# Performance work log

Hardware: AMD Instinct MI355X
Metric: run time of the kernel (lower is better)

## Reference

```python
import jax, jax.numpy as jnp
import numpy as np

B, S, E = 4, 2048, 1024


def setup_inputs() -> dict:
    key = jax.random.key(0)
    ks = jax.random.split(key, 7)
    sc = 1.0 / np.sqrt(E)
    return {
        "embedded": jax.random.normal(ks[0], (B, S, E), dtype=jnp.float32),
        "Wk": jax.random.normal(ks[1], (E, E), dtype=jnp.float32) * sc,
        "bk": jax.random.normal(ks[2], (E,), dtype=jnp.float32) * 0.01,
        "Wq": jax.random.normal(ks[3], (E, E), dtype=jnp.float32) * sc,
        "bq": jax.random.normal(ks[4], (E,), dtype=jnp.float32) * 0.01,
        "Wv": jax.random.normal(ks[5], (E, E), dtype=jnp.float32) * sc,
        "bv": jax.random.normal(ks[6], (E,), dtype=jnp.float32) * 0.01,
    }


def reference(embedded, Wk, bk, Wq, bq, Wv, bv):
    # embedded: [B, S, E]
    K = embedded @ Wk.T + bk  # [B,S,E]
    Q = embedded @ Wq.T + bq
    V = embedded @ Wv.T + bv
    seq_len = K.shape[1]
    # score[b,i,j] = K_i . Q_j, scaled by 1/sqrt(seq_len) (as in original)
    scores = jnp.einsum('bie,bje->bij', K, Q) / jnp.sqrt(jnp.asarray(seq_len, K.dtype))
    # softmax over dim=-2 -> over the key index i
    W = jax.nn.softmax(scores, axis=-2)  # [B,S,S]
    # Y = (V^T @ W)^T -> Y[b,j,d] = sum_i V[b,i,d] * W[b,i,j]
    Y = jnp.einsum('bid,bij->bjd', V, W)  # [B,S,E]
    return Y
```

## Files before the change

### kernel.cpp

```cpp
#include <hip/hip_runtime.h>
#include <hip/hip_bf16.h>


typedef __bf16 bf16x8 __attribute__((ext_vector_type(8)));
typedef float  f32x4  __attribute__((ext_vector_type(4)));

__device__ __forceinline__ unsigned short f2bf(float f) {
    unsigned int u = __float_as_uint(f);
    u = (u + 0x7FFFu + ((u >> 16) & 1u)) >> 16;
    return (unsigned short)u;
}

__global__ __launch_bounds__(256)
void cvt_all(const float* __restrict__ X,  const float* __restrict__ Wq,
             const float* __restrict__ Wk, const float* __restrict__ Wv,
             unsigned short* __restrict__ Xb,  unsigned short* __restrict__ Wqb,
             unsigned short* __restrict__ Wkb, unsigned short* __restrict__ Wvb,
             float* __restrict__ l) {
    long i = (long)blockIdx.x * 256 + threadIdx.x;
    if (i < 8192) l[i] = 0.0f;
    const float* src; unsigned short* dst; long off;
    if (i < 2097152L) { src = X; dst = Xb; off = i; }
    else {
        long j = i - 2097152L;
        int w = (int)(j >> 18);
        off = j & 262143L;
        src = (w == 0) ? Wq : (w == 1) ? Wk : Wv;
        dst = (w == 0) ? Wqb : (w == 1) ? Wkb : Wvb;
    }
    float4 v = reinterpret_cast<const float4*>(src)[off];
    ushort4 o;
    o.x = f2bf(v.x); o.y = f2bf(v.y); o.z = f2bf(v.z); o.w = f2bf(v.w);
    reinterpret_cast<ushort4*>(dst)[off] = o;
}


#define VMW(N) asm volatile("s_waitcnt vmcnt(" #N ")" ::: "memory")

#define PIPE_DECLS                                                          \
    const int tid  = threadIdx.x;                                           \
    const int wave = tid >> 6;                                              \
    const int lane = tid & 63;                                              \
    const int quad = lane >> 4;                                             \
    const int lr   = lane & 15;                                             \
    const int wvm  = wave >> 2;                           \
    const int wvn  = wave & 3;                            \
    const int rd_off = (lr >> 1) * 64 + (lr & 1) * 32                       \
                     + ((quad ^ ((lr >> 1) & 3)) << 3);                     \
    const int stg_rl = wave * 16 + ((lane >> 3) << 1) + ((lane >> 2) & 1);  \
    const int stg_c  = (((lane & 3) ^ ((lane >> 3) & 3)) << 3);

#define ST1(base, LD, kcol, dst, c)                                         \
    __builtin_amdgcn_global_load_lds(                                       \
        (const __attribute__((address_space(1))) void*)                     \
            ((base) + (long)(c) * 128 * (LD) + (kcol)),                     \
        (__attribute__((address_space(3))) void*)(&lds[(dst) + (c) * 4096 + wave * 512]), \
        16, 0, 0)

#define PHASE(bs, h, mh, IH_, STG, WAITS)                                   \
    {                                                                       \
        if ((mh) == 0) {                                                    \
            _Pragma("unroll")                                               \
            for (int j = 0; j < 4; ++j)                                     \
                bfr[j] = __builtin_bit_cast(bf16x8,                         \
                    *reinterpret_cast<const uint4*>(                        \
                        &lds[BOFF(bs, h) + (wvn * 4 + j) * 512 + rd_off])); \
        }                                                                   \
        bf16x8 af[IH_];                                                     \
        _Pragma("unroll")                                                   \
        for (int i = 0; i < (IH_); ++i)                                     \
            af[i] = __builtin_bit_cast(bf16x8,                              \
                *reinterpret_cast<const uint4*>(                            \
                    &lds[AOFF(bs, h) + (wvm * 2 * (IH_) + (mh) * (IH_) + i) * 512 + rd_off])); \
        STG;                                                                \
        WAITS;                                                              \
        __builtin_amdgcn_s_barrier();                                       \
        __builtin_amdgcn_s_setprio(1);                                      \
        _Pragma("unroll")                                                   \
        for (int i = 0; i < (IH_); ++i)                                     \
            _Pragma("unroll")                                               \
            for (int j = 0; j < 4; ++j)                                     \
                acc[(mh) * (IH_) + i][j] = __builtin_amdgcn_mfma_f32_16x16x32_bf16( \
                    af[i], bfr[j], acc[(mh) * (IH_) + i][j], 0, 0, 0);      \
        __builtin_amdgcn_s_setprio(0);                                      \
        __builtin_amdgcn_s_barrier();                                       \
    }

#define RUN_PIPELINE(IH_, NT_, WAITST)                                      \
    f32x4 acc[2 * (IH_)][4] = {};                                           \
    bf16x8 bfr[4];                                                          \
    SA(0, 0, 0); SB(0, 0, 0); SA(0, 1, 0); SB(0, 1, 0); SA(1, 0, 1); SB(1, 0, 1); \
    WAITST;                                                                 \
    __builtin_amdgcn_s_barrier();                                           \
    _Pragma("unroll 1")                                                     \
    for (int it = 0; it < (NT_) / 2 - 1; ++it) {                            \
        const int tb = 2 * it;                                              \
        PHASE(0, 0, 0, IH_, SA(tb + 1, 1, 1), )                             \
        PHASE(0, 0, 1, IH_, SB(tb + 1, 1, 1), )                             \
        PHASE(0, 1, 0, IH_, SA(tb + 2, 0, 0), )                             \
        PHASE(0, 1, 1, IH_, SB(tb + 2, 0, 0), WAITST)                       \
        PHASE(1, 0, 0, IH_, SA(tb + 2, 1, 0), )                             \
        PHASE(1, 0, 1, IH_, SB(tb + 2, 1, 0), )                             \
        PHASE(1, 1, 0, IH_, SA(tb + 3, 0, 1), )                             \
        PHASE(1, 1, 1, IH_, SB(tb + 3, 0, 1), WAITST)                       \
    }                                                                       \
    PHASE(0, 0, 0, IH_, SA((NT_) - 1, 1, 1), )                              \
    PHASE(0, 0, 1, IH_, SB((NT_) - 1, 1, 1), )                              \
    PHASE(0, 1, 0, IH_, , )                                                 \
    PHASE(0, 1, 1, IH_, , WAITST)                                           \
    PHASE(1, 0, 0, IH_, , )                                                 \
    PHASE(1, 0, 1, IH_, , VMW(0))                                           \
    PHASE(1, 1, 0, IH_, , )                                                 \
    PHASE(1, 1, 1, IH_, , )

#define AOFF(b, h) ((b) * 32768 + (h) * 8192)
#define BOFF(b, h) ((b) * 32768 + 16384 + (h) * 8192)
#define SA(tt, h, b) { ST1(aBase, 1024, (tt) * 64 + (h) * 32, AOFF(b, h), 0); \
                       ST1(aBase, 1024, (tt) * 64 + (h) * 32, AOFF(b, h), 1); }
#define SB(tt, h, b) { ST1(bBase, 1024, (tt) * 64 + (h) * 32, BOFF(b, h), 0); \
                       ST1(bBase, 1024, (tt) * 64 + (h) * 32, BOFF(b, h), 1); }

__global__ __launch_bounds__(512, 2)
void gemm_qkv(const unsigned short* __restrict__ Xb,
              const unsigned short* __restrict__ Wqb,
              const unsigned short* __restrict__ Wkb,
              const unsigned short* __restrict__ Wvb,
              const float* __restrict__ bq, const float* __restrict__ bk,
              const float* __restrict__ bv_,
              unsigned short* __restrict__ Qb, unsigned short* __restrict__ Kb,
              unsigned short* __restrict__ Vt)
{
    __shared__ __align__(16) unsigned short lds[65536];

    const int id = blockIdx.x;
    const int g  = id & 7;
    const int u  = id >> 3;
    const int z  = u >> 4;
    const int w  = u & 15;
    const int m0 = (g * 4 + (w >> 2)) * 256;
    const int n0 = (w & 3) * 256;

    const unsigned short* Aptr = Xb;
    const unsigned short* Bptr = (z == 0) ? Wqb : (z == 1) ? Wkb : Wvb;
    const float* bias          = (z == 0) ? bq  : (z == 1) ? bk  : bv_;

    PIPE_DECLS
    const unsigned short* aBase = Aptr + (long)(m0 + stg_rl) * 1024 + stg_c;
    const unsigned short* bBase = Bptr + (long)(n0 + stg_rl) * 1024 + stg_c;

    RUN_PIPELINE(4, 16, VMW(4))

#pragma unroll
    for (int j = 0; j < 4; ++j) {
        const int n = n0 + wvn * 64 + j * 16 + lr;
        const float bvv = bias[n];
#pragma unroll
        for (int i = 0; i < 8; ++i) {
            const int mbase = m0 + wvm * 128 + i * 16 + quad * 4;
            if (z < 2) {
                unsigned short* C = (z == 0) ? Qb : Kb;
#pragma unroll
                for (int r = 0; r < 4; ++r)
                    C[(long)(mbase + r) * 1024 + n] = f2bf(acc[i][j][r] + bvv);
            } else {
                ushort4 o;
                o.x = f2bf(acc[i][j][0] + bvv);
                o.y = f2bf(acc[i][j][1] + bvv);
                o.z = f2bf(acc[i][j][2] + bvv);
                o.w = f2bf(acc[i][j][3] + bvv);
                long boff = (long)(mbase >> 11) * (1024L * 2048) + (long)n * 2048 + (mbase & 2047);
                *reinterpret_cast<ushort4*>(Vt + boff) = o;
            }
        }
    }
}

__global__ __launch_bounds__(512, 2)
void gemm_scores(const unsigned short* __restrict__ Q,
                 const unsigned short* __restrict__ Kp,
                 unsigned short* __restrict__ P, float* __restrict__ l,
                 float scale)
{
    __shared__ __align__(16) unsigned short lds[65536];

    const int id = blockIdx.x;
    const int g  = id & 7;
    const int u  = id >> 3;
    const int bz = g >> 1;
    const int m0 = ((g & 1) * 4 + (u & 3)) * 256;
    const int n0 = (u >> 2) * 256;

    const unsigned short* Aptr = Q  + (long)bz * 2048 * 1024;
    const unsigned short* Bptr = Kp + (long)bz * 2048 * 1024;
    unsigned short* Pb = P + (long)bz * 2048 * 2048;
    float* lb = l + bz * 2048;

    PIPE_DECLS
    const unsigned short* aBase = Aptr + (long)(m0 + stg_rl) * 1024 + stg_c;
    const unsigned short* bBase = Bptr + (long)(n0 + stg_rl) * 1024 + stg_c;

    RUN_PIPELINE(4, 16, VMW(4))

#pragma unroll
    for (int i = 0; i < 8; ++i) {
#pragma unroll
        for (int r = 0; r < 4; ++r) {
            const int m = m0 + wvm * 128 + i * 16 + quad * 4 + r;
            float psum = 0.0f;
#pragma unroll
            for (int j = 0; j < 4; ++j) {
                const float p = __expf(acc[i][j][r] * scale);
                psum += p;
                Pb[(long)m * 2048 + (n0 + wvn * 64 + j * 16 + lr)] = f2bf(p);
            }
#pragma unroll
            for (int o = 1; o < 16; o <<= 1) psum += __shfl_xor(psum, o, 64);
            if (lr == 0) atomicAdd(&lb[m], psum);
        }
    }
}

#undef SA
#undef SB
#undef AOFF
#undef BOFF

#define AOFF(b, h) ((b) * 24576 + (h) * 4096)
#define BOFF(b, h) ((b) * 24576 + 8192 + (h) * 8192)
#define SA(tt, h, b) { ST1(aBase, 2048, (tt) * 64 + (h) * 32, AOFF(b, h), 0); }
#define SB(tt, h, b) { ST1(bBase, 2048, (tt) * 64 + (h) * 32, BOFF(b, h), 0); \
                       ST1(bBase, 2048, (tt) * 64 + (h) * 32, BOFF(b, h), 1); }

__global__ __launch_bounds__(512, 2)
void gemm_y(const unsigned short* __restrict__ P,
            const unsigned short* __restrict__ Vt,
            const float* __restrict__ l, float* __restrict__ out)
{
    __shared__ __align__(16) unsigned short lds[49152];

    const int id = blockIdx.x;
    const int g  = id & 7;
    const int u  = id >> 3;
    const int bz = g >> 1;
    const int m0 = ((g & 1) * 8 + (u & 7)) * 128;
    const int n0 = (u >> 3) * 256;

    const unsigned short* Aptr = P  + (long)bz * 2048 * 2048;
    const unsigned short* Bptr = Vt + (long)bz * 1024 * 2048;
    const float* lb = l + bz * 2048;
    float* C = out + (long)bz * 2048 * 1024;

    PIPE_DECLS
    const unsigned short* aBase = Aptr + (long)(m0 + stg_rl) * 2048 + stg_c;
    const unsigned short* bBase = Bptr + (long)(n0 + stg_rl) * 2048 + stg_c;

    RUN_PIPELINE(2, 32, VMW(3))

    float linv[4][4];
#pragma unroll
    for (int i = 0; i < 4; ++i)
#pragma unroll
        for (int r = 0; r < 4; ++r)
            linv[i][r] = 1.0f / lb[m0 + wvm * 64 + i * 16 + quad * 4 + r];

#pragma unroll
    for (int j = 0; j < 4; ++j) {
        const int n = n0 + wvn * 64 + j * 16 + lr;
#pragma unroll
        for (int i = 0; i < 4; ++i) {
            const int mbase = m0 + wvm * 64 + i * 16 + quad * 4;
#pragma unroll
            for (int r = 0; r < 4; ++r)
                C[(long)(mbase + r) * 1024 + n] = acc[i][j][r] * linv[i][r];
        }
    }
}

#undef SA
#undef SB
#undef AOFF
#undef BOFF

extern "C" void kernel_launch(void* const* d_in, const int* in_sizes, int n_in,
                              void* d_out, int out_size, void* d_ws, size_t ws_size,
                              hipStream_t stream) {
    const float* X  = (const float*)d_in[0];
    const float* Wk = (const float*)d_in[1];
    const float* bk = (const float*)d_in[2];
    const float* Wq = (const float*)d_in[3];
    const float* bq = (const float*)d_in[4];
    const float* Wv = (const float*)d_in[5];
    const float* bv = (const float*)d_in[6];
    float* out = (float*)d_out;

    const size_t MB = 1024 * 1024;
    if (ws_size < 80 * MB) return;

    char* ws = (char*)d_ws;
    unsigned short* Vt  = (unsigned short*)(ws);
    unsigned short* P   = (unsigned short*)(ws + 16 * MB);
    unsigned short* Xbf = (unsigned short*)(ws + 16 * MB);
    float*          l   = (float*)(ws + 48 * MB);
    unsigned short* Wqb = (unsigned short*)(ws + 49 * MB);
    unsigned short* Wkb = (unsigned short*)(ws + 51 * MB);
    unsigned short* Wvb = (unsigned short*)(ws + 53 * MB);
    unsigned short* Qb = (unsigned short*)d_out;
    unsigned short* Kb = Qb + 8192L * 1024;

    cvt_all<<<2883584 / 256, dim3(256), 0, stream>>>(X, Wq, Wk, Wv, Xbf, Wqb, Wkb, Wvb, l);

    gemm_qkv<<<384, dim3(512), 0, stream>>>(Xbf, Wqb, Wkb, Wvb, bq, bk, bv, Qb, Kb, Vt);

    gemm_scores<<<256, dim3(512), 0, stream>>>(Qb, Kb, P, l, 0.022097086912079608f);

    gemm_y<<<256, dim3(512), 0, stream>>>(P, Vt, l, out);
}
```

Measured before the change: 247.6 us.

## Replace QKV pipelined GEMM with 128x128 direct-to-LDS tiled kernel

The QKV projection GEMM moves from a 256x256-tile, 512-thread, deeply software-pipelined kernel to a simpler 128x128-tile, 256-thread kernel. The new kernel stages A and B through LDS with global_load_lds and an XOR swizzle, and launches 1536 blocks instead of 384. That gives more blocks per CU and better load balance across the 256 CUs, in exchange for lower per-tile data reuse and no multi-stage prefetch. Separately, the shared PHASE macro used by the remaining GEMMs gains an explicit lgkmcnt(0) wait and a sched_barrier before the MFMA block.

```diff
diff --git a/kernel.cpp b/kernel.cpp
--- a/kernel.cpp
+++ b/kernel.cpp
@@ -32,6 +32,111 @@
     ushort4 o;
     o.x = f2bf(v.x); o.y = f2bf(v.y); o.z = f2bf(v.z); o.w = f2bf(v.w);
     reinterpret_cast<ushort4*>(dst)[off] = o;
+}
+
+#define GEMM_DECLS                                                      \
+    const int t    = threadIdx.x;                                       \
+    const int wave = t >> 6;                                            \
+    const int lane = t & 63;                                            \
+    const int quad = lane >> 4;                                         \
+    const int lr   = lane & 15;                                         \
+    const int wm   = (wave >> 1) * 64;                                  \
+    const int wn   = (wave & 1) * 64;                                   \
+    const int sx   = lr & 7;                                            \
+    const int lrow = lane >> 3;                                         \
+    const int gch  = ((lane & 7) ^ (lrow & 7)) * 8;
+
+#define GEMM_KLOOP(Aptr, Bptr, LDA, LDB)                                \
+    for (int k0 = 0; k0 < K; k0 += 64) {                                \
+        _Pragma("unroll")                                               \
+        for (int r = 0; r < 4; ++r) {                                   \
+            const int rowb = wave * 8 + r * 32;                         \
+            const int row  = rowb + lrow;                               \
+            const long goffA = (long)(m0 + row) * (LDA) + k0 + gch;     \
+            const long goffB = (long)(n0 + row) * (LDB) + k0 + gch;     \
+            __builtin_amdgcn_global_load_lds(                           \
+                (const __attribute__((address_space(1))) void*)((Aptr) + goffA), \
+                (__attribute__((address_space(3))) void*)(&lsA[rowb * 64]), 16, 0, 0); \
+            __builtin_amdgcn_global_load_lds(                           \
+                (const __attribute__((address_space(1))) void*)((Bptr) + goffB), \
+                (__attribute__((address_space(3))) void*)(&lsB[rowb * 64]), 16, 0, 0); \
+        }                                                               \
+        __syncthreads();                                                \
+        _Pragma("unroll")                                               \
+        for (int h = 0; h < 2; ++h) {                                   \
+            const int cp = ((h * 4 + quad) ^ sx) * 8;                   \
+            bf16x8 af[4], bfr[4];                                       \
+            _Pragma("unroll")                                           \
+            for (int i = 0; i < 4; ++i) {                               \
+                af[i]  = __builtin_bit_cast(bf16x8,                     \
+                          *reinterpret_cast<const uint4*>(&lsA[(wm + i * 16 + lr) * 64 + cp])); \
+                bfr[i] = __builtin_bit_cast(bf16x8,                     \
+                          *reinterpret_cast<const uint4*>(&lsB[(wn + i * 16 + lr) * 64 + cp])); \
+            }                                                           \
+            _Pragma("unroll")                                           \
+            for (int i = 0; i < 4; ++i)                                 \
+                _Pragma("unroll")                                       \
+                for (int j = 0; j < 4; ++j)                             \
+                    acc[i][j] = __builtin_amdgcn_mfma_f32_16x16x32_bf16(af[i], bfr[j], acc[i][j], 0, 0, 0); \
+        }                                                               \
+        __syncthreads();                                                \
+    }
+
+__global__ __launch_bounds__(256, 2)
+void gemm_qkv(const unsigned short* __restrict__ Xb,
+              const unsigned short* __restrict__ Wqb,
+              const unsigned short* __restrict__ Wkb,
+              const unsigned short* __restrict__ Wvb,
+              const float* __restrict__ bq, const float* __restrict__ bk,
+              const float* __restrict__ bv_,
+              unsigned short* __restrict__ Qb, unsigned short* __restrict__ Kb,
+              unsigned short* __restrict__ Vt)
+{
+    __shared__ unsigned short lsA[128 * 64];
+    __shared__ unsigned short lsB[128 * 64];
+
+    const int id  = blockIdx.x;
+    const int g   = id & 7;
+    const int jj  = id >> 3;
+    const int xx  = jj & 7;
+    const int yin = (jj >> 3) & 7;
+    const int z   = jj >> 6;
+
+    const unsigned short* A = Xb;
+    const unsigned short* B = (z == 0) ? Wqb : (z == 1) ? Wkb : Wvb;
+    const float* bias       = (z == 0) ? bq  : (z == 1) ? bk  : bv_;
+
+    const int n0 = xx * 128;
+    const int m0 = (g * 8 + yin) * 128;
+    const int K = 1024;
+
+    GEMM_DECLS
+    f32x4 acc[4][4] = {};
+    GEMM_KLOOP(A, B, 1024, 1024)
+
+#pragma unroll
+    for (int j = 0; j < 4; ++j) {
+        const int n = n0 + wn + j * 16 + lr;
+        const float bvv = bias[n];
+#pragma unroll
+        for (int i = 0; i < 4; ++i) {
+            const int mbase = m0 + wm + i * 16 + quad * 4;
+            if (z < 2) {
+                unsigned short* C = (z == 0) ? Qb : Kb;
+#pragma unroll
+                for (int r = 0; r < 4; ++r)
+                    C[(long)(mbase + r) * 1024 + n] = f2bf(acc[i][j][r] + bvv);
+            } else {
+                ushort4 o;
+                o.x = f2bf(acc[i][j][0] + bvv);
+                o.y = f2bf(acc[i][j][1] + bvv);
+                o.z = f2bf(acc[i][j][2] + bvv);
+                o.w = f2bf(acc[i][j][3] + bvv);
+                long boff = (long)(mbase >> 11) * (1024L * 2048) + (long)n * 2048 + (mbase & 2047);
+                *reinterpret_cast<ushort4*>(Vt + boff) = o;
+            }
+        }
+    }
 }
 
 
@@ -75,6 +180,8 @@
         STG;                                                                \
         WAITS;                                                              \
         __builtin_amdgcn_s_barrier();                                       \
+        asm volatile("s_waitcnt lgkmcnt(0)");                               \
+        __builtin_amdgcn_sched_barrier(0);                                  \
         __builtin_amdgcn_s_setprio(1);                                      \
         _Pragma("unroll")                                                   \
         for (int i = 0; i < (IH_); ++i)                                     \
@@ -121,61 +228,6 @@
                        ST1(bBase, 1024, (tt) * 64 + (h) * 32, BOFF(b, h), 1); }
 
 __global__ __launch_bounds__(512, 2)
-void gemm_qkv(const unsigned short* __restrict__ Xb,
-              const unsigned short* __restrict__ Wqb,
-              const unsigned short* __restrict__ Wkb,
-              const unsigned short* __restrict__ Wvb,
-              const float* __restrict__ bq, const float* __restrict__ bk,
-              const float* __restrict__ bv_,
-              unsigned short* __restrict__ Qb, unsigned short* __restrict__ Kb,
-              unsigned short* __restrict__ Vt)
-{
-    __shared__ __align__(16) unsigned short lds[65536];
-
-    const int id = blockIdx.x;
-    const int g  = id & 7;
-    const int u  = id >> 3;
-    const int z  = u >> 4;
-    const int w  = u & 15;
-    const int m0 = (g * 4 + (w >> 2)) * 256;
-    const int n0 = (w & 3) * 256;
-
-    const unsigned short* Aptr = Xb;
-    const unsigned short* Bptr = (z == 0) ? Wqb : (z == 1) ? Wkb : Wvb;
-    const float* bias          = (z == 0) ? bq  : (z == 1) ? bk  : bv_;
-
-    PIPE_DECLS
-    const unsigned short* aBase = Aptr + (long)(m0 + stg_rl) * 1024 + stg_c;
-    const unsigned short* bBase = Bptr + (long)(n0 + stg_rl) * 1024 + stg_c;
-
-    RUN_PIPELINE(4, 16, VMW(4))
-
-#pragma unroll
-    for (int j = 0; j < 4; ++j) {
-        const int n = n0 + wvn * 64 + j * 16 + lr;
-        const float bvv = bias[n];
-#pragma unroll
-        for (int i = 0; i < 8; ++i) {
-            const int mbase = m0 + wvm * 128 + i * 16 + quad * 4;
-            if (z < 2) {
-                unsigned short* C = (z == 0) ? Qb : Kb;
-#pragma unroll
-                for (int r = 0; r < 4; ++r)
-                    C[(long)(mbase + r) * 1024 + n] = f2bf(acc[i][j][r] + bvv);
-            } else {
-                ushort4 o;
-                o.x = f2bf(acc[i][j][0] + bvv);
-                o.y = f2bf(acc[i][j][1] + bvv);
-                o.z = f2bf(acc[i][j][2] + bvv);
-                o.w = f2bf(acc[i][j][3] + bvv);
-                long boff = (long)(mbase >> 11) * (1024L * 2048) + (long)n * 2048 + (mbase & 2047);
-                *reinterpret_cast<ushort4*>(Vt + boff) = o;
-            }
-        }
-    }
-}
-
-__global__ __launch_bounds__(512, 2)
 void gemm_scores(const unsigned short* __restrict__ Q,
                  const unsigned short* __restrict__ Kp,
                  unsigned short* __restrict__ P, float* __restrict__ l,
@@ -309,7 +361,7 @@
 
     cvt_all<<<2883584 / 256, dim3(256), 0, stream>>>(X, Wq, Wk, Wv, Xbf, Wqb, Wkb, Wvb, l);
 
-    gemm_qkv<<<384, dim3(512), 0, stream>>>(Xbf, Wqb, Wkb, Wvb, bq, bk, bv, Qb, Kb, Vt);
+    gemm_qkv<<<1536, dim3(256), 0, stream>>>(Xbf, Wqb, Wkb, Wvb, bq, bk, bv, Qb, Kb, Vt);
 
     gemm_scores<<<256, dim3(512), 0, stream>>>(Qb, Kb, P, l, 0.022097086912079608f);
 
```

New measurement: 225.4 us. -8.9%, faster.
